# Performance work log

Hardware: AMD Instinct MI355X
Metric: run time of the kernel (lower is better)

Reference implementation:

```python
import itertools
import jax, jax.numpy as jnp
import numpy as np

# ---- config (mirrors init_kwargs) ----
BS = 8; H = 120; W = 160
RES = 5; ZRES = 5
MAP_SIZE_CM = 2400 // 2          # global_downscaling = 2 -> 1200 cm
VR = 100                          # vision_range
FOV = 79.0
NSEM = 16
CAT_THR = 5.0; EXP_THR = 1.0; MAP_THR = 1.0
AGENT_H = 0.88 * 100.0            # camera height in cm
MAX_H = int(360 / ZRES)           # 72
MIN_H = int(-40 / ZRES)           # -8
MAP_DIM = MAP_SIZE_CM // RES      # 240
XC = (W - 1.0) / 2.0
ZC = (H - 1.0) / 2.0
FL = (W / 2.0) / np.tan(np.deg2rad(FOV / 2.0))
D2R = 1.0 / 57.29577951308232


def splat_feat_nd(init_grid, feat, coords):
    """Trilinear splat-scatter. init_grid: (B,F,*gd); feat: (B,F,P); coords: (B,ndim,P) in [-1,1]."""
    B, Fc = init_grid.shape[:2]
    gd = init_grid.shape[2:]
    n = len(gd)
    grid_flat = init_grid.reshape(B, Fc, -1)
    pos_d, wts_d = [], []
    for d in range(n):
        pos = coords[:, d:d + 1, :] * (gd[d] / 2.0) + gd[d] / 2.0  # (B,1,P)
        pd, wd = [], []
        for ix in (0, 1):
            pos_ix = jnp.floor(pos) + ix
            safe = ((pos_ix > 0) & (pos_ix < gd[d])).astype(pos.dtype)
            wd.append((1.0 - jnp.abs(pos - pos_ix)) * safe)
            pd.append((pos_ix * safe).astype(jnp.int32))
        pos_d.append(pd); wts_d.append(wd)
    bidx = jnp.arange(B)[:, None, None]
    fidx = jnp.arange(Fc)[None, :, None]
    for comb in itertools.product((0, 1), repeat=n):
        idx = jnp.zeros_like(pos_d[0][0])
        w = jnp.ones_like(wts_d[0][0])
        for d in range(n):
            idx = idx * gd[d] + pos_d[d][comb[d]]
            w = w * wts_d[d][comb[d]]
        grid_flat = grid_flat.at[bidx, fidx, idx].add(feat * w)
    return jnp.round(grid_flat).reshape(init_grid.shape)


def affine_grid(theta, Ho, Wo):
    """torch F.affine_grid with align_corners=True. theta: (B,2,3) -> (B,Ho,Wo,2)."""
    xs = jnp.linspace(-1.0, 1.0, Wo)
    ys = jnp.linspace(-1.0, 1.0, Ho)
    Xg, Yg = jnp.meshgrid(xs, ys)
    base = jnp.stack([Xg, Yg, jnp.ones_like(Xg)], -1)  # (Ho,Wo,3)
    return jnp.einsum('hwk,bjk->bhwj', base, theta)


def grid_sample(img, grid):
    """Bilinear grid_sample, align_corners=True, zero padding. img: (B,C,Hi,Wi); grid: (B,Ho,Wo,2)."""
    B, C, Hi, Wi = img.shape
    x = (grid[..., 0] + 1.0) * (Wi - 1) / 2.0
    y = (grid[..., 1] + 1.0) * (Hi - 1) / 2.0
    x0 = jnp.floor(x); y0 = jnp.floor(y)
    bidx = jnp.arange(B)[:, None, None, None]
    cidx = jnp.arange(C)[None, :, None, None]

    def tap(ix, iy, w):
        valid = ((ix >= 0) & (ix < Wi) & (iy >= 0) & (iy < Hi)).astype(img.dtype)
        ixc = jnp.clip(ix, 0, Wi - 1).astype(jnp.int32)
        iyc = jnp.clip(iy, 0, Hi - 1).astype(jnp.int32)
        v = img[bidx, cidx, iyc[:, None], ixc[:, None]]  # (B,C,Ho,Wo)
        return v * (w * valid)[:, None]

    out = tap(x0, y0, (x0 + 1 - x) * (y0 + 1 - y))
    out = out + tap(x0 + 1, y0, (x - x0) * (y0 + 1 - y))
    out = out + tap(x0, y0 + 1, (x0 + 1 - x) * (y - y0))
    out = out + tap(x0 + 1, y0 + 1, (x - x0) * (y - y0))
    return out


def _forward(obs, pose_obs, maps_last, poses_last):
    B, c = obs.shape[0], obs.shape[1]
    depth = obs[:, 3]  # (B,H,W), cm

    # point cloud from depth (du.get_point_cloud_from_z_t, du_scale=1)
    gx = jnp.broadcast_to(jnp.arange(W, dtype=depth.dtype)[None, :], (H, W))
    gz = jnp.broadcast_to(jnp.arange(H - 1, -1, -1, dtype=depth.dtype)[:, None], (H, W))
    X = (gx - XC) * depth / FL
    Z = (gz - ZC) * depth / FL
    pc = jnp.stack([X, depth, Z], axis=-1)  # (B,H,W,3)

    # camera elevation rotation about x-axis (view_angles default to 0)
    elev = jnp.zeros((B,), depth.dtype)
    ce, se = jnp.cos(elev), jnp.sin(elev)
    z0 = jnp.zeros_like(ce); o1 = jnp.ones_like(ce)
    Rx = jnp.stack([o1, z0, z0, z0, ce, -se, z0, se, ce], -1).reshape(B, 3, 3)
    pc = jnp.einsum('bhwk,bjk->bhwj', pc, Rx)
    pc = pc.at[..., 2].add(AGENT_H)

    # shift pose: rotate about z by (pi/2 - pi/2) = 0, translate x by vr*res//2
    ang = np.pi / 2.0 - np.pi / 2.0
    Rz = jnp.array([[np.cos(ang), -np.sin(ang), 0.0],
                    [np.sin(ang), np.cos(ang), 0.0],
                    [0.0, 0.0, 1.0]], depth.dtype)
    pc = jnp.einsum('bhwk,jk->bhwj', pc, Rz)
    pc = pc.at[..., 0].add(VR * RES // 2)

    # normalize to [-1,1] voxel coords
    xs = (pc[..., 0] / RES - VR // 2.0) / VR * 2.0
    ys = (pc[..., 1] / RES - VR // 2.0) / VR * 2.0
    zs = (pc[..., 2] / ZRES - (MAX_H + MIN_H) // 2.0) / (MAX_H - MIN_H) * 2.0
    coords = jnp.stack([xs, ys, zs], 1).reshape(B, 3, H * W)

    # feat: channel 0 = ones (occupancy), rest = semantic masks (AvgPool2d(1) = identity)
    feat = jnp.concatenate([jnp.ones((B, 1, H * W), obs.dtype),
                            obs[:, 4:].reshape(B, NSEM, H * W)], axis=1)

    init_grid = jnp.zeros((B, 1 + NSEM, VR, VR, MAX_H - MIN_H), obs.dtype)
    voxels = splat_feat_nd(init_grid, feat, coords).swapaxes(2, 3)

    min_z = int(5 / ZRES - MIN_H)                  # 9
    max_z = int((AGENT_H + 1 + 50) / ZRES - MIN_H)  # 35
    agent_height_proj = voxels[..., min_z:max_z].sum(4)
    all_height_proj = voxels.sum(4)

    fp_map_pred = jnp.clip(agent_height_proj[:, 0:1] / MAP_THR, 0.0, 1.0)
    fp_exp_pred = jnp.clip(all_height_proj[:, 0:1] / EXP_THR, 0.0, 1.0)

    agent_view = jnp.zeros((B, c, MAP_DIM, MAP_DIM), obs.dtype)
    x1 = MAP_SIZE_CM // (RES * 2) - VR // 2; x2 = x1 + VR
    y1 = MAP_SIZE_CM // (RES * 2); y2 = y1 + VR
    agent_view = agent_view.at[:, 0:1, y1:y2, x1:x2].set(fp_map_pred)
    agent_view = agent_view.at[:, 1:2, y1:y2, x1:x2].set(fp_exp_pred)
    agent_view = agent_view.at[:, 4:, y1:y2, x1:x2].set(
        jnp.clip(agent_height_proj[:, 1:] / CAT_THR, 0.0, 1.0))
    # cat_pred_threshold > 5.0 branch is False (threshold == 5.0)

    # pose update (note: torch mutates poses_last in place -> pose_pred aliases current_poses)
    th = poses_last[:, 2] * D2R
    ny = poses_last[:, 1] + pose_obs[:, 0] * jnp.sin(th) + pose_obs[:, 1] * jnp.cos(th)
    nx = poses_last[:, 0] + pose_obs[:, 0] * jnp.cos(th) - pose_obs[:, 1] * jnp.sin(th)
    nt = poses_last[:, 2] + pose_obs[:, 2] * 57.29577951308232
    nt = jnp.fmod(nt - 180.0, 360.0) + 180.0
    nt = jnp.fmod(nt + 180.0, 360.0) - 180.0
    current_poses = jnp.stack([nx, ny, nt], 1)

    st = jax.lax.stop_gradient(current_poses)  # .clone().detach()
    half = MAP_SIZE_CM // (RES * 2)
    st_xy = -(st[:, :2] * 100.0 / RES - half) / half
    st_t = 90.0 - st[:, 2]
    cos_t = jnp.cos(st_t * np.pi / 180.0); sin_t = jnp.sin(st_t * np.pi / 180.0)
    z0 = jnp.zeros_like(cos_t); o1 = jnp.ones_like(cos_t)
    theta1 = jnp.stack([jnp.stack([cos_t, -sin_t, z0], 1),
                        jnp.stack([sin_t, cos_t, z0], 1)], 1)
    theta2 = jnp.stack([jnp.stack([o1, z0, st_xy[:, 0]], 1),
                        jnp.stack([z0, o1, st_xy[:, 1]], 1)], 1)
    rot_grid = affine_grid(theta1, MAP_DIM, MAP_DIM)
    trans_grid = affine_grid(theta2, MAP_DIM, MAP_DIM)
    rotated = grid_sample(agent_view, rot_grid)
    translated = grid_sample(rotated, trans_grid)

    map_pred = jnp.maximum(maps_last, translated)
    return (fp_map_pred, map_pred, current_poses, current_poses)


def setup_inputs() -> dict:
    key = jax.random.key(0)
    k1, k2, k3, k4, k5, k6 = jax.random.split(key, 6)
    obs = jax.random.uniform(k1, (BS, 4 + NSEM, H, W), jnp.float32)
    depth = 50.0 + 300.0 * jax.random.uniform(k2, (BS, H, W), jnp.float32)  # cm
    obs = obs.at[:, 3].set(depth)
    pose_obs = 0.1 * jax.random.normal(k3, (BS, 3), jnp.float32)
    maps_last = jax.random.uniform(k4, (BS, 4 + NSEM, MAP_DIM, MAP_DIM), jnp.float32)
    xy = 4.0 + 4.0 * jax.random.uniform(k5, (BS, 2), jnp.float32)  # meters, inside 12m map
    th = 360.0 * jax.random.uniform(k6, (BS, 1), jnp.float32) - 180.0
    poses_last = jnp.concatenate([xy, th], 1)
    return {"obs": obs, "pose_obs": pose_obs, "maps_last": maps_last, "poses_last": poses_last}


def reference(obs, pose_obs, maps_last, poses_last):
    return _forward(obs, pose_obs, maps_last, poses_last)
```

## Files before the change

kernel.cpp:

```cpp
#include <hip/hip_runtime.h>
#include <math.h>

#define NB 8
#define NH 120
#define NW 160
#define HW (NH*NW)
#define NSEM 16
#define NCH 20
#define VR 100
#define NZ 80
#define NZP 40
#define ZLO 9
#define ZHI 35
#define NZS (ZHI-ZLO)
#define MD 240
#define PC 20
#define YW 64
#define YOFF 8
#define QS0    256.0f
#define QS0INV 0.00390625f
#define QS2    8.0f
#define QS2INV 0.125f
#define PXB 120
#define ACCS 124

__device__ __forceinline__ float clamp01(float v){ return fminf(fmaxf(v, 0.0f), 1.0f); }

struct SplatCoord {
    float wx0, wx1, wy0, wy1, wz0, wz1;
    int   xi0, xi1, yi0, yi1, zi0, zi1;
};
__device__ __forceinline__ void compute_coord(float d, int h, int w, float fl, SplatCoord& sc) {
    float X = ((float)w - 79.5f) * d / fl;
    float Z = ((float)(119 - h) - 59.5f) * d / fl;
    float pcx = X + 250.0f;
    float pcy = d;
    float pcz = Z + 88.0f;
    float posx = ((pcx/5.0f - 50.0f)/100.0f*2.0f)*50.0f + 50.0f;
    float posy = ((pcy/5.0f - 50.0f)/100.0f*2.0f)*50.0f + 50.0f;
    float posz = ((pcz/5.0f - 32.0f)/80.0f*2.0f)*40.0f + 40.0f;
    float f;
    f = floorf(posx);
    { float pi = f;        bool s = (pi > 0.0f) && (pi < 100.0f);
      sc.wx0 = s ? (1.0f - fabsf(posx - pi)) : 0.0f; sc.xi0 = s ? (int)pi : 0; }
    { float pi = f + 1.0f; bool s = (pi > 0.0f) && (pi < 100.0f);
      sc.wx1 = s ? (1.0f - fabsf(posx - pi)) : 0.0f; sc.xi1 = s ? (int)pi : 0; }
    f = floorf(posy);
    { float pi = f;        bool s = (pi > 0.0f) && (pi < 100.0f);
      sc.wy0 = s ? (1.0f - fabsf(posy - pi)) : 0.0f; sc.yi0 = s ? (int)pi : 0; }
    { float pi = f + 1.0f; bool s = (pi > 0.0f) && (pi < 100.0f);
      sc.wy1 = s ? (1.0f - fabsf(posy - pi)) : 0.0f; sc.yi1 = s ? (int)pi : 0; }
    f = floorf(posz);
    { float pi = f;        bool s = (pi > 0.0f) && (pi < 80.0f);
      sc.wz0 = s ? (1.0f - fabsf(posz - pi)) : 0.0f; sc.zi0 = s ? (int)pi : 0; }
    { float pi = f + 1.0f; bool s = (pi > 0.0f) && (pi < 80.0f);
      sc.wz1 = s ? (1.0f - fabsf(posz - pi)) : 0.0f; sc.zi1 = s ? (int)pi : 0; }
}

__global__ void zero_k(uint4* __restrict__ vox0q4, uint4* __restrict__ voxS4) {
    int b = blockIdx.x & 7;
    int i = ((blockIdx.x >> 3) << 8) + threadIdx.x;
    const uint4 z = make_uint4(0u, 0u, 0u, 0u);
    if (i < 64000) {
        vox0q4[(size_t)b*64000 + i] = z;
    } else {
        voxS4[(size_t)b*166400 + (i - 64000)] = z;
    }
}

__global__ void pose_k(const float* __restrict__ pose_obs,
                       const float* __restrict__ poses_last,
                       float* __restrict__ out2, float* __restrict__ out3,
                       float* __restrict__ aux) {
    int b = threadIdx.x;
    if (b >= NB) return;
    const float D2R = 0.017453292519943295f;
    float th = poses_last[b*3+2] * D2R;
    float s = sinf(th), c = cosf(th);
    float ny = poses_last[b*3+1] + pose_obs[b*3+0]*s + pose_obs[b*3+1]*c;
    float nx = poses_last[b*3+0] + pose_obs[b*3+0]*c - pose_obs[b*3+1]*s;
    float nt = poses_last[b*3+2] + pose_obs[b*3+2]*57.29577951308232f;
    nt = fmodf(nt - 180.0f, 360.0f) + 180.0f;
    nt = fmodf(nt + 180.0f, 360.0f) - 180.0f;
    out2[b*3+0] = nx; out2[b*3+1] = ny; out2[b*3+2] = nt;
    out3[b*3+0] = nx; out3[b*3+1] = ny; out3[b*3+2] = nt;
    float stt = 90.0f - nt;
    float rad = stt * D2R;
    aux[b*4+0] = cosf(rad);
    aux[b*4+1] = sinf(rad);
    aux[b*4+2] = -(nx*100.0f/5.0f - 120.0f)/120.0f;
    aux[b*4+3] = -(ny*100.0f/5.0f - 120.0f)/120.0f;
}

__global__ void splat_k(const float* __restrict__ obs, unsigned* __restrict__ vox0q,
                        unsigned* __restrict__ voxS, float fl) {
    int b = blockIdx.x & 7;
    int idx = ((blockIdx.x >> 3) << 8) + threadIdx.x;
    if (idx >= HW*4) return;
    int k = idx & 3; int p = idx >> 2;
    int h = p / NW, w = p % NW;
    const float* ob = obs + (size_t)b*NCH*HW;
    float d = ob[3*HW + p];
    SplatCoord sc;
    compute_coord(d, h, w, fl, sc);

    {
        float wxy = ((k & 1) ? sc.wx1 : sc.wx0) * ((k >> 1) ? sc.wy1 : sc.wy0);
        int   xiv = (k & 1) ? sc.xi1 : sc.xi0;
        unsigned ywi = (unsigned)(((k >> 1) ? sc.yi1 : sc.yi0) - YOFF);
        if (wxy != 0.0f && ywi < YW) {
            unsigned q0 = __float2uint_rn(wxy*sc.wz0*QS0);
            unsigned q1 = __float2uint_rn(wxy*sc.wz1*QS0);
            if (q0 | q1) {
                int z0 = sc.zi0, z1 = sc.zi1;
                size_t rowcol = (size_t)ywi*VR + xiv;
                if (q0 && q1 && !(z0 & 1)) {
                    atomicAdd(&vox0q[((size_t)(b*NZP + (z0 >> 1))*YW*VR) + rowcol], q0 | (q1 << 16));
                } else {
                    if (q0) atomicAdd(&vox0q[((size_t)(b*NZP + (z0 >> 1))*YW*VR) + rowcol],
                                      (z0 & 1) ? (q0 << 16) : q0);
                    if (q1) atomicAdd(&vox0q[((size_t)(b*NZP + (z1 >> 1))*YW*VR) + rowcol],
                                      (z1 & 1) ? (q1 << 16) : q1);
                }
            }
        }
    }

    float f0 = ob[(4 + 4*k + 0)*HW + p];
    float f1 = ob[(4 + 4*k + 1)*HW + p];
    float f2 = ob[(4 + 4*k + 2)*HW + p];
    float f3 = ob[(4 + 4*k + 3)*HW + p];
    #pragma unroll
    for (int cz = 0; cz < 2; cz++) {
        int z = cz ? sc.zi1 : sc.zi0;
        float wzv = cz ? sc.wz1 : sc.wz0;
        if (z < ZLO || z >= ZHI) continue;
        #pragma unroll
        for (int cy = 0; cy < 2; cy++) {
            float wyz = (cy ? sc.wy1 : sc.wy0) * wzv;
            unsigned ywi = (unsigned)((cy ? sc.yi1 : sc.yi0) - YOFF);
            if (ywi >= YW) continue;
            #pragma unroll
            for (int cx = 0; cx < 2; cx++) {
                float w3 = (cx ? sc.wx1 : sc.wx0) * wyz;
                int xiv = cx ? sc.xi1 : sc.xi0;
                if (w3 == 0.0f) continue;
                unsigned q0 = __float2uint_rn(f0*w3*QS2);
                unsigned q1 = __float2uint_rn(f1*w3*QS2);
                unsigned q2 = __float2uint_rn(f2*w3*QS2);
                unsigned q3 = __float2uint_rn(f3*w3*QS2);
                unsigned val = q0 | (q1 << 8) | (q2 << 16) | (q3 << 24);
                if (val) {
                    size_t addr = (((((size_t)b*NZS + (z-ZLO))*YW + ywi)*VR + xiv)<<2) + k;
                    atomicAdd(&voxS[addr], val);
                }
            }
        }
    }
}

__global__ void proj_k(const unsigned* __restrict__ vox0q, const unsigned* __restrict__ voxS,
                       float* __restrict__ proj, float* __restrict__ out0) {
    int b = blockIdx.x & 7;
    int t2 = ((blockIdx.x >> 3) << 8) + threadIdx.x;
    if (t2 < VR*VR) {
        int r = t2;
        int yy = r / VR;
        float* pb = proj + ((size_t)b*(VR*VR) + r)*PC;
        if (yy < YOFF || yy >= YOFF+YW) {
            out0[(size_t)b*(VR*VR) + r] = 0.0f;
            *reinterpret_cast<float2*>(pb) = make_float2(0.0f, 0.0f);
            return;
        }
        int rw = (yy - YOFF)*VR + (r % VR);
        const unsigned* col = vox0q + (size_t)b*NZP*(YW*VR) + rw;
        float s_all = 0.0f, s_slab = 0.0f;
        #pragma unroll
        for (int zp = 0; zp < NZP; zp++) {
            unsigned v = col[(size_t)zp*(YW*VR)];
            float v0 = rintf((float)(v & 0xFFFFu)*QS0INV);
            float v1 = rintf((float)(v >> 16)*QS0INV);
            s_all += v0 + v1;
            if (zp >= 5 && zp <= 16) s_slab += v0 + v1;
            else if (zp == 4) s_slab += v1;
            else if (zp == 17) s_slab += v0;
        }
        float fpm = clamp01(s_slab);
        float fpe = clamp01(s_all);
        out0[(size_t)b*(VR*VR) + r] = fpm;
        *reinterpret_cast<float2*>(pb) = make_float2(fpm, fpe);
        return;
    }
    int r = t2 - VR*VR;
    if (r >= VR*VR) return;
    int yy = r / VR;
    float* dst = proj + ((size_t)b*(VR*VR) + r)*PC + 4;
    if (yy < YOFF || yy >= YOFF+YW) {
        *reinterpret_cast<float4*>(dst)      = make_float4(0.0f, 0.0f, 0.0f, 0.0f);
        *reinterpret_cast<float4*>(dst + 4)  = make_float4(0.0f, 0.0f, 0.0f, 0.0f);
        *reinterpret_cast<float4*>(dst + 8)  = make_float4(0.0f, 0.0f, 0.0f, 0.0f);
        *reinterpret_cast<float4*>(dst + 12) = make_float4(0.0f, 0.0f, 0.0f, 0.0f);
        return;
    }
    int rw = (yy - YOFF)*VR + (r % VR);
    float a00=0.f,a01=0.f,a02=0.f,a03=0.f, a10=0.f,a11=0.f,a12=0.f,a13=0.f;
    float a20=0.f,a21=0.f,a22=0.f,a23=0.f, a30=0.f,a31=0.f,a32=0.f,a33=0.f;
    #pragma unroll 13
    for (int zs = 0; zs < NZS; zs++) {
        const uint4 v = *reinterpret_cast<const uint4*>(
            voxS + ((((size_t)b*NZS + zs)*(YW*VR) + rw)<<2));
        a00 += rintf((float)( v.x        & 0xFFu)*QS2INV);
        a01 += rintf((float)((v.x >>  8) & 0xFFu)*QS2INV);
        a02 += rintf((float)((v.x >> 16) & 0xFFu)*QS2INV);
        a03 += rintf((float)( v.x >> 24         )*QS2INV);
        a10 += rintf((float)( v.y        & 0xFFu)*QS2INV);
        a11 += rintf((float)((v.y >>  8) & 0xFFu)*QS2INV);
        a12 += rintf((float)((v.y >> 16) & 0xFFu)*QS2INV);
        a13 += rintf((float)( v.y >> 24         )*QS2INV);
        a20 += rintf((float)( v.z        & 0xFFu)*QS2INV);
        a21 += rintf((float)((v.z >>  8) & 0xFFu)*QS2INV);
        a22 += rintf((float)((v.z >> 16) & 0xFFu)*QS2INV);
        a23 += rintf((float)( v.z >> 24         )*QS2INV);
        a30 += rintf((float)( v.w        & 0xFFu)*QS2INV);
        a31 += rintf((float)((v.w >>  8) & 0xFFu)*QS2INV);
        a32 += rintf((float)((v.w >> 16) & 0xFFu)*QS2INV);
        a33 += rintf((float)( v.w >> 24         )*QS2INV);
    }
    *reinterpret_cast<float4*>(dst) = make_float4(
        clamp01(a00/5.0f), clamp01(a01/5.0f), clamp01(a02/5.0f), clamp01(a03/5.0f));
    *reinterpret_cast<float4*>(dst + 4) = make_float4(
        clamp01(a10/5.0f), clamp01(a11/5.0f), clamp01(a12/5.0f), clamp01(a13/5.0f));
    *reinterpret_cast<float4*>(dst + 8) = make_float4(
        clamp01(a20/5.0f), clamp01(a21/5.0f), clamp01(a22/5.0f), clamp01(a23/5.0f));
    *reinterpret_cast<float4*>(dst + 12) = make_float4(
        clamp01(a30/5.0f), clamp01(a31/5.0f), clamp01(a32/5.0f), clamp01(a33/5.0f));
}

__global__ __launch_bounds__(256) void rottrans_k(const float* __restrict__ proj,
                           const float* __restrict__ aux,
                           const float* __restrict__ maps, float* __restrict__ out1) {
    __shared__ unsigned long long s_tap[16*PXB];
    __shared__ float    s_acc[NCH*ACCS];
    __shared__ unsigned s_live[PXB];
    int blk = blockIdx.x;
    int b = blk & 7;
    int rem = blk >> 3;
    int Y = rem % MD;
    int chunk = rem / MD;
    int X0 = chunk * PXB;
    int t = threadIdx.x;

    if (t < PXB) {
        int X = X0 + t;
        float ct = aux[b*4+0], st = aux[b*4+1];
        float tx = aux[b*4+2], ty = aux[b*4+3];
        const float step = 2.0f/239.0f;
        float Xg = (X == MD-1) ? 1.0f : (-1.0f + (float)X*step);
        float Yg = (Y == MD-1) ? 1.0f : (-1.0f + (float)Y*step);
        float x = (Xg + tx + 1.0f)*119.5f;
        float y = (Yg + ty + 1.0f)*119.5f;
        float x0 = floorf(x), y0 = floorf(y);
        unsigned live = 0;
        #pragma unroll
        for (int tt = 0; tt < 4; tt++) {
            float ix = x0 + (float)(tt & 1);
            float iy = y0 + (float)(tt >> 1);
            float wt = ((tt & 1) ? (x - x0) : (x0 + 1.0f - x)) *
                       ((tt >> 1) ? (y - y0) : (y0 + 1.0f - y));
            bool tvalid = (ix >= 0.0f) && (ix < 240.0f) && (iy >= 0.0f) && (iy < 240.0f) && (wt != 0.0f);
            float u = 0.0f, v = 0.0f;
            if (tvalid) {
                int Xi = (int)ix, Yi = (int)iy;
                float Xg2 = (Xi == MD-1) ? 1.0f : (-1.0f + (float)Xi*step);
                float Yg2 = (Yi == MD-1) ? 1.0f : (-1.0f + (float)Yi*step);
                u = ct*Xg2 - st*Yg2;
                v = st*Xg2 + ct*Yg2;
            }
            float x2 = (u + 1.0f)*119.5f;
            float y2 = (v + 1.0f)*119.5f;
            float x20 = floorf(x2), y20 = floorf(y2);
            #pragma unroll
            for (int ii = 0; ii < 4; ii++) {
                float jx = x20 + (float)(ii & 1);
                float jy = y20 + (float)(ii >> 1);
                float w2 = ((ii & 1) ? (x2 - x20) : (x20 + 1.0f - x2)) *
                           ((ii >> 1) ? (y2 - y20) : (y20 + 1.0f - y2));
                bool ivalid = tvalid && (jy >= 120.0f) && (jy < 220.0f) && (jx >= 70.0f) && (jx < 170.0f);
                int slot = tt*4 + ii;
                float w = ivalid ? wt * w2 : 0.0f;
                int  off = ivalid ? (((int)jy - 120)*VR + ((int)jx - 70)) : 0;
                s_tap[slot*PXB + t] = (unsigned long long)(unsigned)off |
                                      ((unsigned long long)__float_as_uint(w) << 32);
                live |= (w != 0.0f) ? 1u : 0u;
            }
        }
        s_live[t] = live;
    }
    __syncthreads();

    const float* pj = proj + (size_t)b*(VR*VR)*PC;
    for (int item = t; item < PXB*10; item += 256) {
        int px = item / 10, c = item % 10;
        float a0 = 0.0f, a1 = 0.0f;
        if (s_live[px]) {
            #pragma unroll
            for (int s = 0; s < 16; s++) {
                unsigned long long tap = s_tap[s*PXB + px];
                float w = __uint_as_float((unsigned)(tap >> 32));
                const float2 v2 = *reinterpret_cast<const float2*>(
                    pj + (size_t)(unsigned)tap*PC + c*2);
                a0 += w*v2.x; a1 += w*v2.y;
            }
        }
        s_acc[(2*c)*ACCS + px]   = a0;
        s_acc[(2*c+1)*ACCS + px] = a1;
    }
    __syncthreads();

    size_t bbase = (size_t)b*NCH*(MD*MD) + (size_t)Y*MD + X0;
    for (int item = t; item < NCH*(PXB/4); item += 256) {
        int ch = item / (PXB/4), pq = item % (PXB/4);
        size_t o = bbase + (size_t)ch*(MD*MD) + pq*4;
        float4 m = *reinterpret_cast<const float4*>(maps + o);
        float4 r;
        if (ch == 2 || ch == 3) {
            r = make_float4(fmaxf(m.x, 0.0f), fmaxf(m.y, 0.0f),
                            fmaxf(m.z, 0.0f), fmaxf(m.w, 0.0f));
        } else {
            const float4 a = *reinterpret_cast<const float4*>(s_acc + ch*ACCS + pq*4);
            r = make_float4(fmaxf(m.x, a.x), fmaxf(m.y, a.y),
                            fmaxf(m.z, a.z), fmaxf(m.w, a.w));
        }
        *reinterpret_cast<float4*>(out1 + o) = r;
    }
}

extern "C" void kernel_launch(void* const* d_in, const int* in_sizes, int n_in,
                              void* d_out, int out_size, void* d_ws, size_t ws_size,
                              hipStream_t stream) {
    const float* obs        = (const float*)d_in[0];
    const float* pose_obs   = (const float*)d_in[1];
    const float* maps_last  = (const float*)d_in[2];
    const float* poses_last = (const float*)d_in[3];
    float* out  = (float*)d_out;
    float* out0 = out;
    float* out1 = out + 80000;
    float* out2 = out + 80000 + 9216000;
    float* out3 = out2 + 24;

    unsigned* vox0q = (unsigned*)d_ws;
    unsigned* voxS  = (unsigned*)d_ws + 2048000;
    float*    proj  = (float*)d_ws + 2048000 + 5324800;
    float*    aux   = proj + 1600000;

    const float FLf = (float)(80.0 / tan(39.5 * M_PI / 180.0));

    zero_k    <<<900*8, 256, 0, stream>>>((uint4*)vox0q, (uint4*)voxS);
    pose_k    <<<1, 64, 0, stream>>>(pose_obs, poses_last, out2, out3, aux);
    splat_k   <<<300*8, 256, 0, stream>>>(obs, vox0q, voxS, FLf);
    proj_k    <<<79*8, 256, 0, stream>>>(vox0q, voxS, proj, out0);
    rottrans_k<<<480*8, 256, 0, stream>>>(proj, aux, maps_last, out1);
}
```

Baseline: 84.69 us.

## Factor translation as uniform fractional shift and sample rotated grid once per row

The translation step is a pure shift, so it is split into an integer offset plus one fractional bilinear weight per batch, computed in the pose kernel. Each block now rotates and samples a 2x121 strip of grid points with 4 taps each, then blends neighbours with the uniform weights. This replaces the 16 gathers per output pixel. The maps_last loads are also hoisted to the kernel start so they overlap with the compute. Shared memory is reused across phases, and the result relies on the shift-invariance assumption matching the float rounding of the reference.

```diff
diff --git a/kernel.cpp b/kernel.cpp
--- a/kernel.cpp
+++ b/kernel.cpp
@@ -23,6 +23,7 @@
 #define QS2INV 0.125f
 #define PXB 120
 #define ACCS 124
+#define GPTS 242
 
 __device__ __forceinline__ float clamp01(float v){ return fminf(fmaxf(v, 0.0f), 1.0f); }
 
@@ -86,10 +87,17 @@
     out3[b*3+0] = nx; out3[b*3+1] = ny; out3[b*3+2] = nt;
     float stt = 90.0f - nt;
     float rad = stt * D2R;
-    aux[b*4+0] = cosf(rad);
-    aux[b*4+1] = sinf(rad);
-    aux[b*4+2] = -(nx*100.0f/5.0f - 120.0f)/120.0f;
-    aux[b*4+3] = -(ny*100.0f/5.0f - 120.0f)/120.0f;
+    float tx = -(nx*100.0f/5.0f - 120.0f)/120.0f;
+    float ty = -(ny*100.0f/5.0f - 120.0f)/120.0f;
+    float dx = tx * 119.5f;
+    float dy = ty * 119.5f;
+    float Kf = floorf(dx), Lf = floorf(dy);
+    aux[b*12+0] = cosf(rad);
+    aux[b*12+1] = sinf(rad);
+    aux[b*12+2] = Kf;
+    aux[b*12+3] = Lf;
+    aux[b*12+4] = dx - Kf;
+    aux[b*12+5] = dy - Lf;
 }
 
 __global__ void splat_k(const float* __restrict__ obs, unsigned* __restrict__ vox0q,
@@ -239,9 +247,12 @@
 __global__ __launch_bounds__(256) void rottrans_k(const float* __restrict__ proj,
                            const float* __restrict__ aux,
                            const float* __restrict__ maps, float* __restrict__ out1) {
-    __shared__ unsigned long long s_tap[16*PXB];
-    __shared__ float    s_acc[NCH*ACCS];
-    __shared__ unsigned s_live[PXB];
+    __shared__ float s_rot[GPTS*20];
+    __shared__ unsigned long long s_mix64[1240];
+    unsigned long long* s_rtap = s_mix64;
+    unsigned* s_glive = (unsigned*)(s_mix64 + GPTS*4);
+    float* s_acc = (float*)s_mix64;
+
     int blk = blockIdx.x;
     int b = blk & 7;
     int rem = blk >> 3;
@@ -250,88 +261,128 @@
     int X0 = chunk * PXB;
     int t = threadIdx.x;
 
-    if (t < PXB) {
-        int X = X0 + t;
-        float ct = aux[b*4+0], st = aux[b*4+1];
-        float tx = aux[b*4+2], ty = aux[b*4+3];
+    float ct = aux[b*12+0], st = aux[b*12+1];
+    int K = (int)aux[b*12+2], L = (int)aux[b*12+3];
+    float fx = aux[b*12+4], fy = aux[b*12+5];
+
+    size_t bbase = (size_t)b*NCH*(MD*MD) + (size_t)Y*MD + X0;
+    int it0 = t, it1 = t + 256, it2 = t + 512;
+    size_t o0 = bbase + (size_t)(it0/30)*(MD*MD) + (it0%30)*4;
+    size_t o1 = bbase + (size_t)(it1/30)*(MD*MD) + (it1%30)*4;
+    float4 m0 = *reinterpret_cast<const float4*>(maps + o0);
+    float4 m1 = *reinterpret_cast<const float4*>(maps + o1);
+    float4 m2 = make_float4(0.f,0.f,0.f,0.f);
+    size_t o2 = 0;
+    if (it2 < PXB/4*NCH) {
+        o2 = bbase + (size_t)(it2/30)*(MD*MD) + (it2%30)*4;
+        m2 = *reinterpret_cast<const float4*>(maps + o2);
+    }
+
+    if (t < GPTS) {
+        int j = (t >= 121) ? 1 : 0;
+        int u = t - j*121;
+        int U = X0 + K + u;
+        int V = Y + L + j;
+        unsigned live = 0;
         const float step = 2.0f/239.0f;
-        float Xg = (X == MD-1) ? 1.0f : (-1.0f + (float)X*step);
-        float Yg = (Y == MD-1) ? 1.0f : (-1.0f + (float)Y*step);
-        float x = (Xg + tx + 1.0f)*119.5f;
-        float y = (Yg + ty + 1.0f)*119.5f;
-        float x0 = floorf(x), y0 = floorf(y);
-        unsigned live = 0;
+        float x2 = 0.0f, y2 = 0.0f;
+        bool inr = (U >= 0) && (U < MD) && (V >= 0) && (V < MD);
+        if (inr) {
+            float Xg2 = (U == MD-1) ? 1.0f : (-1.0f + (float)U*step);
+            float Yg2 = (V == MD-1) ? 1.0f : (-1.0f + (float)V*step);
+            float ur = ct*Xg2 - st*Yg2;
+            float vr = st*Xg2 + ct*Yg2;
+            x2 = (ur + 1.0f)*119.5f;
+            y2 = (vr + 1.0f)*119.5f;
+        }
+        float x20 = floorf(x2), y20 = floorf(y2);
         #pragma unroll
-        for (int tt = 0; tt < 4; tt++) {
-            float ix = x0 + (float)(tt & 1);
-            float iy = y0 + (float)(tt >> 1);
-            float wt = ((tt & 1) ? (x - x0) : (x0 + 1.0f - x)) *
-                       ((tt >> 1) ? (y - y0) : (y0 + 1.0f - y));
-            bool tvalid = (ix >= 0.0f) && (ix < 240.0f) && (iy >= 0.0f) && (iy < 240.0f) && (wt != 0.0f);
-            float u = 0.0f, v = 0.0f;
-            if (tvalid) {
-                int Xi = (int)ix, Yi = (int)iy;
-                float Xg2 = (Xi == MD-1) ? 1.0f : (-1.0f + (float)Xi*step);
-                float Yg2 = (Yi == MD-1) ? 1.0f : (-1.0f + (float)Yi*step);
-                u = ct*Xg2 - st*Yg2;
-                v = st*Xg2 + ct*Yg2;
-            }
-            float x2 = (u + 1.0f)*119.5f;
-            float y2 = (v + 1.0f)*119.5f;
-            float x20 = floorf(x2), y20 = floorf(y2);
+        for (int ii = 0; ii < 4; ii++) {
+            float jx = x20 + (float)(ii & 1);
+            float jy = y20 + (float)(ii >> 1);
+            float w2 = ((ii & 1) ? (x2 - x20) : (x20 + 1.0f - x2)) *
+                       ((ii >> 1) ? (y2 - y20) : (y20 + 1.0f - y2));
+            bool ivalid = inr && (jy >= 120.0f) && (jy < 220.0f) && (jx >= 70.0f) && (jx < 170.0f);
+            float w = ivalid ? w2 : 0.0f;
+            int  off = ivalid ? (((int)jy - 120)*VR + ((int)jx - 70)) : 0;
+            s_rtap[t*4 + ii] = (unsigned long long)(unsigned)off |
+                               ((unsigned long long)__float_as_uint(w) << 32);
+            live |= (w != 0.0f) ? 1u : 0u;
+        }
+        s_glive[t] = live;
+    }
+    __syncthreads();
+
+    const float* pj = proj + (size_t)b*(VR*VR)*PC;
+    for (int item = t; item < GPTS*10; item += 256) {
+        int g = item / 10, c = item % 10;
+        float a0 = 0.0f, a1 = 0.0f;
+        if (s_glive[g]) {
             #pragma unroll
-            for (int ii = 0; ii < 4; ii++) {
-                float jx = x20 + (float)(ii & 1);
-                float jy = y20 + (float)(ii >> 1);
-                float w2 = ((ii & 1) ? (x2 - x20) : (x20 + 1.0f - x2)) *
-                           ((ii >> 1) ? (y2 - y20) : (y20 + 1.0f - y2));
-                bool ivalid = tvalid && (jy >= 120.0f) && (jy < 220.0f) && (jx >= 70.0f) && (jx < 170.0f);
-                int slot = tt*4 + ii;
-                float w = ivalid ? wt * w2 : 0.0f;
-                int  off = ivalid ? (((int)jy - 120)*VR + ((int)jx - 70)) : 0;
-                s_tap[slot*PXB + t] = (unsigned long long)(unsigned)off |
-                                      ((unsigned long long)__float_as_uint(w) << 32);
-                live |= (w != 0.0f) ? 1u : 0u;
-            }
-        }
-        s_live[t] = live;
-    }
-    __syncthreads();
-
-    const float* pj = proj + (size_t)b*(VR*VR)*PC;
-    for (int item = t; item < PXB*10; item += 256) {
-        int px = item / 10, c = item % 10;
-        float a0 = 0.0f, a1 = 0.0f;
-        if (s_live[px]) {
-            #pragma unroll
-            for (int s = 0; s < 16; s++) {
-                unsigned long long tap = s_tap[s*PXB + px];
+            for (int s = 0; s < 4; s++) {
+                unsigned long long tap = s_rtap[g*4 + s];
                 float w = __uint_as_float((unsigned)(tap >> 32));
                 const float2 v2 = *reinterpret_cast<const float2*>(
                     pj + (size_t)(unsigned)tap*PC + c*2);
                 a0 += w*v2.x; a1 += w*v2.y;
             }
         }
-        s_acc[(2*c)*ACCS + px]   = a0;
-        s_acc[(2*c+1)*ACCS + px] = a1;
+        s_rot[g*20 + 2*c]     = a0;
+        s_rot[g*20 + 2*c + 1] = a1;
     }
     __syncthreads();
 
-    size_t bbase = (size_t)b*NCH*(MD*MD) + (size_t)Y*MD + X0;
-    for (int item = t; item < NCH*(PXB/4); item += 256) {
-        int ch = item / (PXB/4), pq = item % (PXB/4);
-        size_t o = bbase + (size_t)ch*(MD*MD) + pq*4;
-        float4 m = *reinterpret_cast<const float4*>(maps + o);
+    float w00 = (1.0f-fx)*(1.0f-fy), w10 = fx*(1.0f-fy);
+    float w01 = (1.0f-fx)*fy,        w11 = fx*fy;
+    for (int item = t; item < PXB*5; item += 256) {
+        int px = item / 5, q = item % 5;
+        const float4 r00 = *reinterpret_cast<const float4*>(s_rot + (px      )*20 + q*4);
+        const float4 r10 = *reinterpret_cast<const float4*>(s_rot + (px + 1  )*20 + q*4);
+        const float4 r01 = *reinterpret_cast<const float4*>(s_rot + (121 + px    )*20 + q*4);
+        const float4 r11 = *reinterpret_cast<const float4*>(s_rot + (121 + px + 1)*20 + q*4);
+        float a0 = w00*r00.x + w10*r10.x + w01*r01.x + w11*r11.x;
+        float a1 = w00*r00.y + w10*r10.y + w01*r01.y + w11*r11.y;
+        float a2 = w00*r00.z + w10*r10.z + w01*r01.z + w11*r11.z;
+        float a3 = w00*r00.w + w10*r10.w + w01*r01.w + w11*r11.w;
+        s_acc[(4*q+0)*ACCS + px] = a0;
+        s_acc[(4*q+1)*ACCS + px] = a1;
+        s_acc[(4*q+2)*ACCS + px] = a2;
+        s_acc[(4*q+3)*ACCS + px] = a3;
+    }
+    __syncthreads();
+
+    {
+        int ch = it0/30, pq = it0%30;
         float4 r;
         if (ch == 2 || ch == 3) {
-            r = make_float4(fmaxf(m.x, 0.0f), fmaxf(m.y, 0.0f),
-                            fmaxf(m.z, 0.0f), fmaxf(m.w, 0.0f));
+            r = make_float4(fmaxf(m0.x,0.f), fmaxf(m0.y,0.f), fmaxf(m0.z,0.f), fmaxf(m0.w,0.f));
         } else {
             const float4 a = *reinterpret_cast<const float4*>(s_acc + ch*ACCS + pq*4);
-            r = make_float4(fmaxf(m.x, a.x), fmaxf(m.y, a.y),
-                            fmaxf(m.z, a.z), fmaxf(m.w, a.w));
-        }
-        *reinterpret_cast<float4*>(out1 + o) = r;
+            r = make_float4(fmaxf(m0.x,a.x), fmaxf(m0.y,a.y), fmaxf(m0.z,a.z), fmaxf(m0.w,a.w));
+        }
+        *reinterpret_cast<float4*>(out1 + o0) = r;
+    }
+    {
+        int ch = it1/30, pq = it1%30;
+        float4 r;
+        if (ch == 2 || ch == 3) {
+            r = make_float4(fmaxf(m1.x,0.f), fmaxf(m1.y,0.f), fmaxf(m1.z,0.f), fmaxf(m1.w,0.f));
+        } else {
+            const float4 a = *reinterpret_cast<const float4*>(s_acc + ch*ACCS + pq*4);
+            r = make_float4(fmaxf(m1.x,a.x), fmaxf(m1.y,a.y), fmaxf(m1.z,a.z), fmaxf(m1.w,a.w));
+        }
+        *reinterpret_cast<float4*>(out1 + o1) = r;
+    }
+    if (it2 < PXB/4*NCH) {
+        int ch = it2/30, pq = it2%30;
+        float4 r;
+        if (ch == 2 || ch == 3) {
+            r = make_float4(fmaxf(m2.x,0.f), fmaxf(m2.y,0.f), fmaxf(m2.z,0.f), fmaxf(m2.w,0.f));
+        } else {
+            const float4 a = *reinterpret_cast<const float4*>(s_acc + ch*ACCS + pq*4);
+            r = make_float4(fmaxf(m2.x,a.x), fmaxf(m2.y,a.y), fmaxf(m2.z,a.z), fmaxf(m2.w,a.w));
+        }
+        *reinterpret_cast<float4*>(out1 + o2) = r;
     }
 }
 
```

Measured after the change: 82.00 us. 3.2% less time.
